# Performance work log

Hardware: AMD Instinct MI355X
Metric: run time of the kernel (lower is better)

Reference implementation:

```python
import jax, jax.numpy as jnp
import numpy as np

# Static config (matches init_kwargs / module defaults)
H = W = 24           # patch grid per image (hardcoded in module)
N = H * W            # 576 patch tokens
B = 64               # batch of anyres patches
D = 1024             # CLIP-ViT-L hidden size
K = 144              # num_tokens_to_keep
TOPN = 2             # top_n_per_region (TOKEN_CONFIGS[128])
DIST_THR = float(np.sqrt(280.0))
PCT = 0.55           # penalty_threshold_percentile (THRE)


def setup_inputs() -> dict:
    key = jax.random.key(0)
    k1, k2, k3 = jax.random.split(key, 3)
    return {
        "hidden_states_for_aggregation": jax.random.normal(k1, (B, N, D), jnp.float32),
        "hidden_states_for_sim": jax.random.normal(k2, (B, N, D), jnp.float32),
        "cls_attention_map": jax.random.uniform(k3, (B, N), jnp.float32),
    }


def _dist_penalty():
    # penalty(i,j) = max(0, 1 - dist2d(i,j)/thr); [N, N]
    ys, xs = jnp.meshgrid(jnp.arange(H), jnp.arange(W), indexing='ij')
    coords = jnp.stack([ys, xs], axis=-1).reshape(-1, 2).astype(jnp.float32)
    diff = coords[:, None, :] - coords[None, :, :]
    dist = jnp.sqrt(jnp.sum(diff * diff, axis=-1))
    return 1.0 - jnp.minimum(dist / DIST_THR, 1.0)


def reference(hidden_states_for_aggregation, hidden_states_for_sim, cls_attention_map):
    metric = cls_attention_map                      # [B, N]
    # --- per-region (2x2) local top-n selection ---
    m2d = metric.reshape(B, H, W)
    # unfold(1,2,2).unfold(2,2,2) -> [B, H/2, W/2, 2, 2], flat to [B, nr, 4]
    regions = m2d.reshape(B, H // 2, 2, W // 2, 2).transpose(0, 1, 3, 2, 4)
    nr_h, nr_w = H // 2, W // 2
    nr = nr_h * nr_w
    regions = regions.reshape(B, nr, 4)
    _, loc_idx = jax.lax.top_k(regions, TOPN)       # [B, nr, TOPN]
    ly, lx = loc_idx // 2, loc_idx % 2
    rid = jnp.arange(nr)[None, :, None]
    gy = (rid // nr_w) * 2 + ly
    gx = (rid % nr_w) * 2 + lx
    cand = (gy * W + gx).reshape(B, -1)             # [B, nr*TOPN]
    # --- global top-K among candidates ---
    cand_scores = jnp.take_along_axis(metric, cand, axis=1)
    _, top_c = jax.lax.top_k(cand_scores, K)
    benchmark_indices = jnp.sort(jnp.take_along_axis(cand, top_c, axis=1), axis=1)  # [B, K]
    # --- similarity with distance penalty ---
    norm = jnp.linalg.norm(hidden_states_for_sim, axis=-1, keepdims=True)
    pn = hidden_states_for_sim / jnp.maximum(norm, 1e-12)
    sim = jnp.einsum('bnd,bmd->bnm', pn, pn)        # [B, N, N]
    agg_w = jax.nn.relu(sim) * _dist_penalty()      # [B, N, N]
    bscores = jnp.take_along_axis(metric, benchmark_indices, axis=1)    # [B, K]
    thr = jnp.quantile(bscores, PCT, axis=1, keepdims=True)
    high = bscores >= thr                            # [B, K]
    one_hot = benchmark_indices[:, :, None] == jnp.arange(N)[None, None, :]  # [B, K, N]
    # rows of high-attn tokens zeroed except their own (self) column
    spm = jnp.where(high[:, :, None] & (~one_hot), 0.0, 1.0)
    bw = jnp.take_along_axis(agg_w, benchmark_indices[:, :, None], axis=1) * spm
    bwn = bw / (jnp.sum(bw, axis=-1, keepdims=True) + 1e-8)
    bwn = jnp.where(one_hot, 1.0, bwn)               # scatter self-weight = 1
    aggregated = jnp.einsum('bkn,bnd->bkd', bwn, hidden_states_for_aggregation)
    return aggregated, benchmark_indices
```

## Files before the change

### kernel.cpp

```cpp
#include <hip/hip_runtime.h>
#include <hip/hip_bf16.h>
#include <stdint.h>

#define B_  64
#define N_  576
#define D_  1024
#define K_  144
#define HW_ 24
#define DIST_THR_F 16.733200530681511f

using bf16x8 = __attribute__((ext_vector_type(8))) short;
using f32x4  = __attribute__((ext_vector_type(4))) float;

__device__ __forceinline__ unsigned short f2bf(float f) {
    unsigned u = __float_as_uint(f);
    u += 0x7fffu + ((u >> 16) & 1u);
    return (unsigned short)(u >> 16);
}

__device__ __forceinline__ void pack8(const float4 a, const float4 b, float& ss,
                                      unsigned short* __restrict__ dst) {
    ss += a.x*a.x + a.y*a.y + a.z*a.z + a.w*a.w
        + b.x*b.x + b.y*b.y + b.z*b.z + b.w*b.w;
    union { bf16x8 v; unsigned short u[8]; } pk;
    pk.u[0] = f2bf(a.x); pk.u[1] = f2bf(a.y); pk.u[2] = f2bf(a.z); pk.u[3] = f2bf(a.w);
    pk.u[4] = f2bf(b.x); pk.u[5] = f2bf(b.y); pk.u[6] = f2bf(b.z); pk.u[7] = f2bf(b.w);
    *reinterpret_cast<bf16x8*>(dst) = pk.v;
}

__global__ __launch_bounds__(256) void k_select(const float* __restrict__ metric,
                                                int* __restrict__ bench_idx,
                                                int* __restrict__ high,
                                                float* __restrict__ out_idx,
                                                float* __restrict__ rowsum) {
    __shared__ float sm[N_];
    __shared__ float sc[512];
    __shared__ int   si[512];
    __shared__ unsigned smask[18];
    __shared__ int   wpref[18];
    __shared__ float thr_s;
    int b = blockIdx.x, tid = threadIdx.x;
    for (int i = tid; i < N_; i += 256) sm[i] = metric[b * N_ + i];
    if (tid < 18) smask[tid] = 0u;
    if (tid < 144) rowsum[b * K_ + tid] = 0.f;
    __syncthreads();
    if (tid < 144) {
        int ry = tid / 12, rx = tid - ry * 12;
        int base = ry * 48 + rx * 2;
        float vv[4] = { sm[base], sm[base + 1], sm[base + 24], sm[base + 25] };
        int   tk[4] = { base, base + 1, base + 24, base + 25 };
        int a0 = 0;
#pragma unroll
        for (int j = 1; j < 4; j++) if (vv[j] > vv[a0]) a0 = j;
        int a1 = -1;
#pragma unroll
        for (int j = 0; j < 4; j++) {
            if (j == a0) continue;
            if (a1 < 0 || vv[j] > vv[a1]) a1 = j;
        }
        sc[2 * tid]     = vv[a0]; si[2 * tid]     = tk[a0];
        sc[2 * tid + 1] = vv[a1]; si[2 * tid + 1] = tk[a1];
    }
    for (int i = 288 + tid; i < 512; i += 256) { sc[i] = -1e30f; si[i] = 0x7fffffff; }
    __syncthreads();
    for (int k = 2; k <= 512; k <<= 1) {
        for (int j = k >> 1; j > 0; j >>= 1) {
#pragma unroll 2
            for (int t = tid; t < 512; t += 256) {
                int ixj = t ^ j;
                if (ixj > t) {
                    float s1 = sc[t], s2 = sc[ixj];
                    int   i1 = si[t], i2 = si[ixj];
                    bool before = (s1 > s2) || (s1 == s2 && i1 < i2);
                    bool up = ((t & k) == 0);
                    if (up ? !before : before) {
                        sc[t] = s2; sc[ixj] = s1; si[t] = i2; si[ixj] = i1;
                    }
                }
            }
            __syncthreads();
        }
    }
    if (tid == 0) {
        float qpos = 0.55f * 143.0f;
        float g = qpos - 78.0f;
        thr_s = sc[65] * (1.0f - g) + sc[64] * g;
    }
    if (tid < 144) atomicOr(&smask[si[tid] >> 5], 1u << (si[tid] & 31));
    __syncthreads();
    if (tid == 0) {
        int acc = 0;
        for (int w = 0; w < 18; w++) { wpref[w] = acc; acc += __popc(smask[w]); }
    }
    __syncthreads();
    if (tid < 144) {
        int tok = si[tid], w = tok >> 5;
        int rank = wpref[w] + __popc(smask[w] & ((1u << (tok & 31)) - 1u));
        bench_idx[b * K_ + rank] = tok;
        high[b * K_ + rank] = (sc[tid] >= thr_s) ? 1 : 0;
        out_idx[b * K_ + rank] = (float)tok;
    }
}

__global__ __launch_bounds__(384) void k_sim5(const float* __restrict__ hs,
                                              const int* __restrict__ bench_idx,
                                              const int* __restrict__ high,
                                              unsigned short* __restrict__ bwn,
                                              float* __restrict__ rowsum) {
    __shared__ unsigned short SM[336 * 64];
    __shared__ float ssL[336];
    __shared__ float rsum[144];
    int bid  = blockIdx.x;
    int xcd  = bid & 7;
    int s    = bid >> 3;
    int ct   = s % 3;
    int b    = (s / 3) * 8 + xcd;
    int tid  = threadIdx.x;
    int w = tid >> 6, lane = tid & 63, g = lane >> 4, r16 = lane & 15;
    int wr = w >> 1, wc = w & 1;

    if (tid < 336) ssL[tid] = 0.f;
    if (tid < 144) rsum[tid] = 0.f;

    const float* base = hs + (size_t)b * N_ * D_;

    const float* gsrc[7];
    int dsoff[7];
#pragma unroll
    for (int q = 0; q < 7; q++) {
        int cid = tid + 384 * q;
        int row = cid >> 3;
        int p   = cid & 7;
        int l   = p ^ (row & 7);
        int tok = (row < 144) ? bench_idx[b * K_ + row] : (ct * 192 + (row - 144));
        gsrc[q]  = base + (size_t)tok * D_ + l * 8;
        dsoff[q] = row * 64 + p * 8;
    }

    float4 fa[7][2];
    float ssp[7] = {0.f, 0.f, 0.f, 0.f, 0.f, 0.f, 0.f};
#pragma unroll
    for (int q = 0; q < 7; q++) {
        fa[q][0] = *(const float4*)(gsrc[q]);
        fa[q][1] = *(const float4*)(gsrc[q] + 4);
    }

    f32x4 acc[3][6] = {};

    for (int t = 0; t < 16; ++t) {
#pragma unroll
        for (int q = 0; q < 7; q++) pack8(fa[q][0], fa[q][1], ssp[q], &SM[dsoff[q]]);
        __syncthreads();
        if (t < 15) {
            int kb = (t + 1) * 64;
#pragma unroll
            for (int q = 0; q < 7; q++) {
                fa[q][0] = *(const float4*)(gsrc[q] + kb);
                fa[q][1] = *(const float4*)(gsrc[q] + kb + 4);
            }
        }
#pragma unroll
        for (int h = 0; h < 2; h++) {
            int ks = h * 4 + g;
            bf16x8 af[3], bf[6];
#pragma unroll
            for (int mi = 0; mi < 3; mi++) {
                int row = wr * 48 + mi * 16 + r16;
                af[mi] = *(const bf16x8*)&SM[row * 64 + (ks ^ (row & 7)) * 8];
            }
#pragma unroll
            for (int nj = 0; nj < 6; nj++) {
                int row = 144 + wc * 96 + nj * 16 + r16;
                bf[nj] = *(const bf16x8*)&SM[row * 64 + (ks ^ (row & 7)) * 8];
            }
#pragma unroll
            for (int mi = 0; mi < 3; mi++)
#pragma unroll
                for (int nj = 0; nj < 6; nj++)
                    acc[mi][nj] = __builtin_amdgcn_mfma_f32_16x16x32_bf16(af[mi], bf[nj], acc[mi][nj], 0, 0, 0);
        }
        __syncthreads();
    }

#pragma unroll
    for (int q = 0; q < 7; q++) {
        int row = (tid + 384 * q) >> 3;
        atomicAdd(&ssL[row], ssp[q]);
    }
    __syncthreads();

    float invB6[6];
#pragma unroll
    for (int nj = 0; nj < 6; nj++)
        invB6[nj] = 1.0f / fmaxf(sqrtf(ssL[144 + wc * 96 + nj * 16 + r16]), 1e-12f);
#pragma unroll
    for (int mi = 0; mi < 3; mi++) {
#pragma unroll
        for (int r = 0; r < 4; r++) {
            int i = wr * 48 + mi * 16 + g * 4 + r;
            int ti = bench_idx[b * K_ + i];
            int hi = high[b * K_ + i];
            float invA = 1.0f / fmaxf(sqrtf(ssL[i]), 1e-12f);
            int y1 = ti / HW_, x1 = ti % HW_;
            unsigned short* prow = bwn + (size_t)(b * K_ + i) * N_;
            float sum6 = 0.f;
            float vals[6];
#pragma unroll
            for (int nj = 0; nj < 6; nj++) {
                int col = ct * 192 + wc * 96 + nj * 16 + r16;
                int y2 = col / HW_, x2 = col % HW_;
                float dy = (float)(y1 - y2), dx = (float)(x1 - x2);
                float dist = sqrtf(dy * dy + dx * dx);
                float pen = 1.0f - fminf(dist / DIST_THR_F, 1.0f);
                float v = fmaxf(acc[mi][nj][r], 0.0f) * invA * invB6[nj] * pen;
                vals[nj] = v;
                sum6 += v;
            }
#pragma unroll
            for (int m = 1; m <= 8; m <<= 1) sum6 += __shfl_xor(sum6, m, 64);
            if (r16 == 0) atomicAdd(&rsum[i], sum6);
#pragma unroll
            for (int nj = 0; nj < 6; nj++) {
                int col = ct * 192 + wc * 96 + nj * 16 + r16;
                unsigned short o = (hi || col == ti) ? (unsigned short)0 : f2bf(vals[nj]);
                prow[col] = o;
            }
        }
    }
    __syncthreads();
    if (tid < 144) atomicAdd(&rowsum[b * K_ + tid], rsum[tid]);
}

__global__ __launch_bounds__(384) void k_agg5(const unsigned short* __restrict__ bwn,
                                              const float* __restrict__ agg,
                                              const int* __restrict__ bench_idx,
                                              const float* __restrict__ rowsum,
                                              float* __restrict__ out) {
    __shared__ unsigned short LA[144 * 64];
    __shared__ unsigned int   LB[256 * 32];
    int bid  = blockIdx.x;
    int xcd  = bid & 7;
    int s    = bid >> 3;
    int dt   = s & 3;
    int b    = (s >> 2) * 8 + xcd;
    int tid  = threadIdx.x;
    int w = tid >> 6, lane = tid & 63, g = lane >> 4, r16 = lane & 15;
    int wr = w >> 1, wc = w & 1;

    const unsigned short* asrc[3];
    int adso[3];
#pragma unroll
    for (int q = 0; q < 3; q++) {
        int cid = tid + 384 * q;
        int row = cid >> 3, p = cid & 7, l = p ^ (row & 7);
        asrc[q] = bwn + (size_t)(b * K_ + row) * N_ + l * 8;
        adso[q] = row * 64 + p * 8;
    }
    const float* bbase = agg + (size_t)b * N_ * D_ + dt * 256 + lane * 4;

    bf16x8 areg[3];
    float4 breg[6][2];
#pragma unroll
    for (int q = 0; q < 3; q++) areg[q] = *(const bf16x8*)(asrc[q]);
#pragma unroll
    for (int u = 0; u < 6; u++) {
        int pp = w + 6 * u;
        if (pp < 32) {
            breg[u][0] = *(const float4*)(bbase + (size_t)(2 * pp) * D_);
            breg[u][1] = *(const float4*)(bbase + (size_t)(2 * pp + 1) * D_);
        }
    }

    f32x4 acc[3][8] = {};

    for (int t = 0; t < 9; ++t) {
#pragma unroll
        for (int q = 0; q < 3; q++) *(bf16x8*)&LA[adso[q]] = areg[q];
#pragma unroll
        for (int u = 0; u < 6; u++) {
            int pp = w + 6 * u;
            if (pp < 32) {
                float a0[4] = { breg[u][0].x, breg[u][0].y, breg[u][0].z, breg[u][0].w };
                float a1[4] = { breg[u][1].x, breg[u][1].y, breg[u][1].z, breg[u][1].w };
                int js = pp >> 2;
#pragma unroll
                for (int c = 0; c < 4; c++) {
                    int d = lane * 4 + c;
                    int sw = (js ^ (d & 7) ^ ((d >> 3) & 7)) & 7;
                    unsigned pk = (unsigned)f2bf(a0[c]) | ((unsigned)f2bf(a1[c]) << 16);
                    LB[d * 32 + sw * 4 + (pp & 3)] = pk;
                }
            }
        }
        __syncthreads();
        if (t < 8) {
            int kb = (t + 1) * 64;
#pragma unroll
            for (int q = 0; q < 3; q++) areg[q] = *(const bf16x8*)(asrc[q] + kb);
#pragma unroll
            for (int u = 0; u < 6; u++) {
                int pp = w + 6 * u;
                if (pp < 32) {
                    breg[u][0] = *(const float4*)(bbase + (size_t)(kb + 2 * pp) * D_);
                    breg[u][1] = *(const float4*)(bbase + (size_t)(kb + 2 * pp + 1) * D_);
                }
            }
        }
#pragma unroll
        for (int h = 0; h < 2; h++) {
            int ks = h * 4 + g;
            bf16x8 af[3], bf[8];
#pragma unroll
            for (int mi = 0; mi < 3; mi++) {
                int row = wr * 48 + mi * 16 + r16;
                af[mi] = *(const bf16x8*)&LA[row * 64 + (ks ^ (row & 7)) * 8];
            }
#pragma unroll
            for (int nj = 0; nj < 8; nj++) {
                int d = wc * 128 + nj * 16 + r16;
                int sw = (ks ^ (d & 7) ^ ((d >> 3) & 7)) & 7;
                bf[nj] = *(const bf16x8*)&LB[d * 32 + sw * 4];
            }
#pragma unroll
            for (int mi = 0; mi < 3; mi++)
#pragma unroll
                for (int nj = 0; nj < 8; nj++)
                    acc[mi][nj] = __builtin_amdgcn_mfma_f32_16x16x32_bf16(af[mi], bf[nj], acc[mi][nj], 0, 0, 0);
        }
        __syncthreads();
    }

#pragma unroll
    for (int mi = 0; mi < 3; mi++) {
#pragma unroll
        for (int r = 0; r < 4; r++) {
            int i = wr * 48 + mi * 16 + g * 4 + r;
            float S = rowsum[b * K_ + i];
            float sc = 1.0f / (S + 1e-8f);
            int ti = bench_idx[b * K_ + i];
            const float* selfrow = agg + (size_t)(b * N_ + ti) * D_ + dt * 256 + wc * 128;
            float* orow = out + (size_t)(b * K_ + i) * D_ + dt * 256 + wc * 128;
#pragma unroll
            for (int nj = 0; nj < 8; nj++)
                orow[nj * 16 + r16] = acc[mi][nj][r] * sc + selfrow[nj * 16 + r16];
        }
    }
}

extern "C" void kernel_launch(void* const* d_in, const int* in_sizes, int n_in,
                              void* d_out, int out_size, void* d_ws, size_t ws_size,
                              hipStream_t stream) {
    const float* hs_agg = (const float*)d_in[0];
    const float* hs_sim = (const float*)d_in[1];
    const float* metric = (const float*)d_in[2];
    float* out = (float*)d_out;
    char* ws = (char*)d_ws;

    const size_t BWN_BYTES = (size_t)B_ * K_ * N_ * 2;
    unsigned short* bwn = (unsigned short*)ws;
    int*   bench_idx = (int*)(ws + BWN_BYTES);
    int*   high      = (int*)(ws + BWN_BYTES + (size_t)B_ * K_ * 4);
    float* rowsum    = (float*)(ws + BWN_BYTES + (size_t)B_ * K_ * 8);
    float* out_idx   = out + (size_t)B_ * K_ * D_;

    hipLaunchKernelGGL(k_select, dim3(B_),     dim3(256), 0, stream, metric, bench_idx, high, out_idx, rowsum);
    hipLaunchKernelGGL(k_sim5,   dim3(B_ * 3), dim3(384), 0, stream, hs_sim, bench_idx, high, bwn, rowsum);
    hipLaunchKernelGGL(k_agg5,   dim3(B_ * 4), dim3(384), 0, stream, bwn, hs_agg, bench_idx, rowsum, out);
}
```

Measured before the change: 129.6 us.

## Precompute normalized bf16 copy of sim hidden states in a separate kernel

Adds a pre-pass kernel that L2-normalizes each row of hidden_states_for_sim and writes it as bf16 to workspace. The similarity kernel then loads bf16 directly, with no per-tile fp32->bf16 packing, sum-of-squares accumulation or norm scaling in its epilogue. This halves global read traffic in the MFMA kernel, which reloads the 144 benchmark rows once for each of its 3 column tiles. The cost is a full fp32 read plus bf16 write of the 151MB tensor and one extra kernel launch. Numerics change slightly because normalization now happens before bf16 rounding.

```diff
diff --git a/kernel.cpp b/kernel.cpp
--- a/kernel.cpp
+++ b/kernel.cpp
@@ -18,14 +18,29 @@
     return (unsigned short)(u >> 16);
 }
 
-__device__ __forceinline__ void pack8(const float4 a, const float4 b, float& ss,
-                                      unsigned short* __restrict__ dst) {
-    ss += a.x*a.x + a.y*a.y + a.z*a.z + a.w*a.w
-        + b.x*b.x + b.y*b.y + b.z*b.z + b.w*b.w;
-    union { bf16x8 v; unsigned short u[8]; } pk;
-    pk.u[0] = f2bf(a.x); pk.u[1] = f2bf(a.y); pk.u[2] = f2bf(a.z); pk.u[3] = f2bf(a.w);
-    pk.u[4] = f2bf(b.x); pk.u[5] = f2bf(b.y); pk.u[6] = f2bf(b.z); pk.u[7] = f2bf(b.w);
-    *reinterpret_cast<bf16x8*>(dst) = pk.v;
+__global__ __launch_bounds__(256) void k_normcast(const float* __restrict__ x,
+                                                  unsigned short* __restrict__ pn) {
+    int row  = blockIdx.x * 4 + (threadIdx.x >> 6);
+    int lane = threadIdx.x & 63;
+    const float4* src = reinterpret_cast<const float4*>(x + (size_t)row * D_);
+    float4 v[4];
+    float ss = 0.f;
+#pragma unroll
+    for (int q = 0; q < 4; q++) {
+        v[q] = src[lane + 64 * q];
+        ss += v[q].x * v[q].x + v[q].y * v[q].y + v[q].z * v[q].z + v[q].w * v[q].w;
+    }
+#pragma unroll
+    for (int m = 32; m >= 1; m >>= 1) ss += __shfl_xor(ss, m, 64);
+    float inv = 1.0f / fmaxf(sqrtf(ss), 1e-12f);
+    ushort4* dst = reinterpret_cast<ushort4*>(pn + (size_t)row * D_);
+#pragma unroll
+    for (int q = 0; q < 4; q++) {
+        ushort4 o;
+        o.x = f2bf(v[q].x * inv); o.y = f2bf(v[q].y * inv);
+        o.z = f2bf(v[q].z * inv); o.w = f2bf(v[q].w * inv);
+        dst[lane + 64 * q] = o;
+    }
 }
 
 __global__ __launch_bounds__(256) void k_select(const float* __restrict__ metric,
@@ -102,13 +117,12 @@
     }
 }
 
-__global__ __launch_bounds__(384) void k_sim5(const float* __restrict__ hs,
+__global__ __launch_bounds__(384) void k_sim8(const unsigned short* __restrict__ pn,
                                               const int* __restrict__ bench_idx,
                                               const int* __restrict__ high,
                                               unsigned short* __restrict__ bwn,
                                               float* __restrict__ rowsum) {
     __shared__ unsigned short SM[336 * 64];
-    __shared__ float ssL[336];
     __shared__ float rsum[144];
     int bid  = blockIdx.x;
     int xcd  = bid & 7;
@@ -119,12 +133,11 @@
     int w = tid >> 6, lane = tid & 63, g = lane >> 4, r16 = lane & 15;
     int wr = w >> 1, wc = w & 1;
 
-    if (tid < 336) ssL[tid] = 0.f;
     if (tid < 144) rsum[tid] = 0.f;
 
-    const float* base = hs + (size_t)b * N_ * D_;
-
-    const float* gsrc[7];
+    const unsigned short* pnb = pn + (size_t)b * N_ * D_;
+
+    const unsigned short* gsrc[7];
     int dsoff[7];
 #pragma unroll
     for (int q = 0; q < 7; q++) {
@@ -133,31 +146,24 @@
         int p   = cid & 7;
         int l   = p ^ (row & 7);
         int tok = (row < 144) ? bench_idx[b * K_ + row] : (ct * 192 + (row - 144));
-        gsrc[q]  = base + (size_t)tok * D_ + l * 8;
+        gsrc[q]  = pnb + (size_t)tok * D_ + l * 8;
         dsoff[q] = row * 64 + p * 8;
     }
 
-    float4 fa[7][2];
-    float ssp[7] = {0.f, 0.f, 0.f, 0.f, 0.f, 0.f, 0.f};
-#pragma unroll
-    for (int q = 0; q < 7; q++) {
-        fa[q][0] = *(const float4*)(gsrc[q]);
-        fa[q][1] = *(const float4*)(gsrc[q] + 4);
-    }
+    bf16x8 sreg[7];
+#pragma unroll
+    for (int q = 0; q < 7; q++) sreg[q] = *(const bf16x8*)(gsrc[q]);
 
     f32x4 acc[3][6] = {};
 
     for (int t = 0; t < 16; ++t) {
 #pragma unroll
-        for (int q = 0; q < 7; q++) pack8(fa[q][0], fa[q][1], ssp[q], &SM[dsoff[q]]);
+        for (int q = 0; q < 7; q++) *(bf16x8*)&SM[dsoff[q]] = sreg[q];
         __syncthreads();
         if (t < 15) {
             int kb = (t + 1) * 64;
 #pragma unroll
-            for (int q = 0; q < 7; q++) {
-                fa[q][0] = *(const float4*)(gsrc[q] + kb);
-                fa[q][1] = *(const float4*)(gsrc[q] + kb + 4);
-            }
+            for (int q = 0; q < 7; q++) sreg[q] = *(const bf16x8*)(gsrc[q] + kb);
         }
 #pragma unroll
         for (int h = 0; h < 2; h++) {
@@ -182,17 +188,6 @@
         __syncthreads();
     }
 
-#pragma unroll
-    for (int q = 0; q < 7; q++) {
-        int row = (tid + 384 * q) >> 3;
-        atomicAdd(&ssL[row], ssp[q]);
-    }
-    __syncthreads();
-
-    float invB6[6];
-#pragma unroll
-    for (int nj = 0; nj < 6; nj++)
-        invB6[nj] = 1.0f / fmaxf(sqrtf(ssL[144 + wc * 96 + nj * 16 + r16]), 1e-12f);
 #pragma unroll
     for (int mi = 0; mi < 3; mi++) {
 #pragma unroll
@@ -200,11 +195,10 @@
             int i = wr * 48 + mi * 16 + g * 4 + r;
             int ti = bench_idx[b * K_ + i];
             int hi = high[b * K_ + i];
-            float invA = 1.0f / fmaxf(sqrtf(ssL[i]), 1e-12f);
             int y1 = ti / HW_, x1 = ti % HW_;
             unsigned short* prow = bwn + (size_t)(b * K_ + i) * N_;
+            float vals[6];
             float sum6 = 0.f;
-            float vals[6];
 #pragma unroll
             for (int nj = 0; nj < 6; nj++) {
                 int col = ct * 192 + wc * 96 + nj * 16 + r16;
@@ -212,7 +206,7 @@
                 float dy = (float)(y1 - y2), dx = (float)(x1 - x2);
                 float dist = sqrtf(dy * dy + dx * dx);
                 float pen = 1.0f - fminf(dist / DIST_THR_F, 1.0f);
-                float v = fmaxf(acc[mi][nj][r], 0.0f) * invA * invB6[nj] * pen;
+                float v = fmaxf(acc[mi][nj][r], 0.0f) * pen;
                 vals[nj] = v;
                 sum6 += v;
             }
@@ -356,14 +350,17 @@
     float* out = (float*)d_out;
     char* ws = (char*)d_ws;
 
+    const size_t PN_BYTES  = (size_t)B_ * N_ * D_ * 2;
     const size_t BWN_BYTES = (size_t)B_ * K_ * N_ * 2;
-    unsigned short* bwn = (unsigned short*)ws;
-    int*   bench_idx = (int*)(ws + BWN_BYTES);
-    int*   high      = (int*)(ws + BWN_BYTES + (size_t)B_ * K_ * 4);
-    float* rowsum    = (float*)(ws + BWN_BYTES + (size_t)B_ * K_ * 8);
+    unsigned short* pn  = (unsigned short*)ws;
+    unsigned short* bwn = (unsigned short*)(ws + PN_BYTES);
+    int*   bench_idx = (int*)(ws + PN_BYTES + BWN_BYTES);
+    int*   high      = (int*)(ws + PN_BYTES + BWN_BYTES + (size_t)B_ * K_ * 4);
+    float* rowsum    = (float*)(ws + PN_BYTES + BWN_BYTES + (size_t)B_ * K_ * 8);
     float* out_idx   = out + (size_t)B_ * K_ * D_;
 
-    hipLaunchKernelGGL(k_select, dim3(B_),     dim3(256), 0, stream, metric, bench_idx, high, out_idx, rowsum);
-    hipLaunchKernelGGL(k_sim5,   dim3(B_ * 3), dim3(384), 0, stream, hs_sim, bench_idx, high, bwn, rowsum);
-    hipLaunchKernelGGL(k_agg5,   dim3(B_ * 4), dim3(384), 0, stream, bwn, hs_agg, bench_idx, rowsum, out);
-}
+    hipLaunchKernelGGL(k_normcast, dim3((B_ * N_) / 4), dim3(256), 0, stream, hs_sim, pn);
+    hipLaunchKernelGGL(k_select,   dim3(B_),            dim3(256), 0, stream, metric, bench_idx, high, out_idx, rowsum);
+    hipLaunchKernelGGL(k_sim8,     dim3(B_ * 3),        dim3(384), 0, stream, pn, bench_idx, high, bwn, rowsum);
+    hipLaunchKernelGGL(k_agg5,     dim3(B_ * 4),        dim3(384), 0, stream, bwn, hs_agg, bench_idx, rowsum, out);
+}
```

New measurement: 136.3 us. +5.1%, slower.
